# Kernel optimization log

Measured on AMD Instinct MI355X. Metric: run time of the kernel, lower is better.

## Reference

```python
import jax, jax.numpy as jnp
import numpy as np

N = 8192
D = 512
H = 256
K_TOPK = 21  # k + 1 with k = 20
EPS_NORM = 1e-12
EPS_DEG = 1e-10


def setup_inputs() -> dict:
    key = jax.random.key(0)
    ks = jax.random.split(key, 10)
    s = 0.02  # small init scale so similarities are well-behaved
    return {
        "features": jax.random.normal(ks[0], (N, D), jnp.float32),
        "masked_features": jax.random.normal(ks[1], (N, D), jnp.float32),
        "W1": jax.random.normal(ks[2], (D, D), jnp.float32) * s,
        "b1": jax.random.normal(ks[3], (D,), jnp.float32) * s,
        "W2": jax.random.normal(ks[4], (D, D), jnp.float32) * s,
        "b2": jax.random.normal(ks[5], (D,), jnp.float32) * s,
        "Wg1": jax.random.normal(ks[6], (D, H), jnp.float32) * s,
        "bg1": jax.random.normal(ks[7], (H,), jnp.float32) * s,
        "Wg2": jax.random.normal(ks[8], (H, D), jnp.float32) * s,
        "bg2": jax.random.normal(ks[9], (D,), jnp.float32) * s,
    }


def reference(features, masked_features, W1, b1, W2, b2, Wg1, bg1, Wg2, bg2):
    # ---- graph generator MLP ----
    h = jax.nn.relu(features @ W1 + b1)            # [N, D]
    emb = h @ W2 + b2                              # [N, D]
    norm = jnp.linalg.norm(emb, axis=1, keepdims=True)
    emb = emb / jnp.maximum(norm, EPS_NORM)        # F.normalize(dim=1, p=2)
    sim = emb @ emb.T                              # [N, N] cosine similarity

    # ---- top-k mask (k+1 neighbors), zero diagonal ----
    _, idx = jax.lax.top_k(sim, K_TOPK)            # [N, K]
    rows = jnp.arange(N)[:, None]
    mask = jnp.zeros((N, N), sim.dtype).at[rows, idx].set(1.0)
    mask = mask * (1.0 - jnp.eye(N, dtype=sim.dtype))  # fill_diagonal_(0)
    mask = jax.lax.stop_gradient(mask)
    sim = jax.nn.relu(sim * mask)

    # ---- symmetrize ----
    gen_adj = (sim + sim.T) * 0.5                  # [N, N]

    # ---- degree norm: D^{-1/2} (A + I) D^{-1/2} ----
    A = gen_adj + jnp.eye(N, dtype=gen_adj.dtype)
    inv_sqrt_deg = 1.0 / (jnp.sqrt(A.sum(axis=1)) + EPS_DEG)
    A = inv_sqrt_deg[:, None] * A * inv_sqrt_deg[None, :]

    # ---- two dense GCN hops (dropout inert in eval mode) ----
    h1 = jax.nn.relu(A @ (masked_features @ Wg1 + bg1))  # [N, H]
    h3 = A @ (h1 @ Wg2 + bg2)                            # [N, D]
    return h3, gen_adj
```

## Files before the change

### kernel.cpp

```cpp
#include <hip/hip_runtime.h>
#include <cstdint>
#include <cstddef>

#define NN 8192
#define DD 512
#define HH 256
#define KTOP 21
#define CCAP 192
#define CMIN 48
#define ECAP 224
#define NBIN 1024

typedef __attribute__((ext_vector_type(8))) __bf16 bf16x8;
typedef __attribute__((ext_vector_type(4))) float f32x4;

__device__ __forceinline__ unsigned short f2bf(float x) {
    unsigned u = __float_as_uint(x);
    u += 0x7fffu + ((u >> 16) & 1u);
    return (unsigned short)(u >> 16);
}
__device__ __forceinline__ float bf2f(unsigned short h) {
    return __uint_as_float(((unsigned)h) << 16);
}
__device__ __forceinline__ unsigned ordkey(float x) {
    unsigned b = __float_as_uint(x);
    return b ^ (((int)b >> 31) | 0x80000000u);
}

#define GLD16(gp, lp) __builtin_amdgcn_global_load_lds( \
    (const __attribute__((address_space(1))) unsigned int*)(gp), \
    (__attribute__((address_space(3))) unsigned int*)(lp), 16, 0, 0)

template<bool TRANSB, int ACT>
__global__ __launch_bounds__(256)
void sgemm128(const float* __restrict__ A, const float* __restrict__ B,
              const float* __restrict__ bias, float* __restrict__ C,
              int M, int N, int K) {
    constexpr int BM = 128, BN = 128, BK = 16;
    __shared__ float As[BK][BM + 4];
    __shared__ float Bs[BK][BN + 4];

    const int tiles_n = N / BN;
    const int by = blockIdx.x / tiles_n;
    const int bx = blockIdx.x % tiles_n;
    const int row0 = by * BM, col0 = bx * BN;
    const int tid = threadIdx.x;
    const int tx = tid & 15, ty = tid >> 4;

    float acc[8][8];
#pragma unroll
    for (int m = 0; m < 8; ++m)
#pragma unroll
        for (int n = 0; n < 8; ++n) acc[m][n] = 0.f;

    for (int k0 = 0; k0 < K; k0 += BK) {
#pragma unroll
        for (int l = 0; l < 2; ++l) {
            int f = tid + l * 256;
            int r = f >> 2, c4 = f & 3;
            float4 v = *reinterpret_cast<const float4*>(
                A + (size_t)(row0 + r) * K + k0 + c4 * 4);
            As[c4 * 4 + 0][r] = v.x;
            As[c4 * 4 + 1][r] = v.y;
            As[c4 * 4 + 2][r] = v.z;
            As[c4 * 4 + 3][r] = v.w;
        }
        if (TRANSB) {
#pragma unroll
            for (int l = 0; l < 2; ++l) {
                int f = tid + l * 256;
                int r = f >> 2, c4 = f & 3;
                float4 v = *reinterpret_cast<const float4*>(
                    B + (size_t)(col0 + r) * K + k0 + c4 * 4);
                Bs[c4 * 4 + 0][r] = v.x;
                Bs[c4 * 4 + 1][r] = v.y;
                Bs[c4 * 4 + 2][r] = v.z;
                Bs[c4 * 4 + 3][r] = v.w;
            }
        } else {
#pragma unroll
            for (int l = 0; l < 2; ++l) {
                int f = tid + l * 256;
                int kr = f >> 5, n4 = f & 31;
                *reinterpret_cast<float4*>(&Bs[kr][n4 * 4]) =
                    *reinterpret_cast<const float4*>(
                        B + (size_t)(k0 + kr) * N + col0 + n4 * 4);
            }
        }
        __syncthreads();

#pragma unroll
        for (int kk = 0; kk < BK; ++kk) {
            float a[8], b[8];
            *(float4*)&a[0] = *(const float4*)&As[kk][ty * 8];
            *(float4*)&a[4] = *(const float4*)&As[kk][ty * 8 + 4];
            *(float4*)&b[0] = *(const float4*)&Bs[kk][tx * 8];
            *(float4*)&b[4] = *(const float4*)&Bs[kk][tx * 8 + 4];
#pragma unroll
            for (int m = 0; m < 8; ++m)
#pragma unroll
                for (int n = 0; n < 8; ++n)
                    acc[m][n] = fmaf(a[m], b[n], acc[m][n]);
        }
        __syncthreads();
    }

    const int crow = row0 + ty * 8;
    const int ccol = col0 + tx * 8;
    float bv[8];
#pragma unroll
    for (int n = 0; n < 8; ++n) bv[n] = bias ? bias[ccol + n] : 0.f;
#pragma unroll
    for (int m = 0; m < 8; ++m) {
        float o[8];
#pragma unroll
        for (int n = 0; n < 8; ++n) {
            float t = acc[m][n] + bv[n];
            if (ACT == 1) t = fmaxf(t, 0.f);
            o[n] = t;
        }
        *reinterpret_cast<float4*>(C + (size_t)(crow + m) * N + ccol)     = *(float4*)&o[0];
        *reinterpret_cast<float4*>(C + (size_t)(crow + m) * N + ccol + 4) = *(float4*)&o[4];
    }
}

__global__ __launch_bounds__(256)
void rownorm_emit_kernel(float* __restrict__ emb, unsigned short* __restrict__ ehi) {
    const int row = blockIdx.x, tid = threadIdx.x;
    float* rp = emb + (size_t)row * DD;
    float v0 = rp[tid], v1 = rp[tid + 256];
    float sum = v0 * v0 + v1 * v1;
#pragma unroll
    for (int off = 32; off > 0; off >>= 1) sum += __shfl_down(sum, off, 64);
    __shared__ float ws[4];
    __shared__ float sc_sh;
    if ((tid & 63) == 0) ws[tid >> 6] = sum;
    __syncthreads();
    if (tid == 0) {
        float n = sqrtf(ws[0] + ws[1] + ws[2] + ws[3]);
        sc_sh = 1.0f / fmaxf(n, 1e-12f);
    }
    __syncthreads();
    float sc = sc_sh;
    v0 *= sc; v1 *= sc;
    rp[tid] = v0;
    rp[tid + 256] = v1;
    ehi[(size_t)row * DD + tid]       = f2bf(v0);
    ehi[(size_t)row * DD + tid + 256] = f2bf(v1);
}

__global__ __launch_bounds__(256)
void split_kernel(const float* __restrict__ e, unsigned short* __restrict__ hi,
                  unsigned short* __restrict__ lo) {
    const int i = (blockIdx.x * 256 + threadIdx.x) * 4;
    float4 v = *reinterpret_cast<const float4*>(e + i);
    ushort4 h, l;
    h.x = f2bf(v.x); l.x = f2bf(v.x - bf2f(h.x));
    h.y = f2bf(v.y); l.y = f2bf(v.y - bf2f(h.y));
    h.z = f2bf(v.z); l.z = f2bf(v.z - bf2f(h.z));
    h.w = f2bf(v.w); l.w = f2bf(v.w - bf2f(h.w));
    *reinterpret_cast<ushort4*>(hi + i) = h;
    *reinterpret_cast<ushort4*>(lo + i) = l;
}

__global__ __launch_bounds__(256)
void wtrans_kernel(const float* __restrict__ W, unsigned short* __restrict__ Thi,
                   unsigned short* __restrict__ Tlo, int K, int N) {
    int t = blockIdx.x * 256 + threadIdx.x;
    if (t >= K * N) return;
    int k = t / N, n = t - k * N;
    float x = W[t];
    unsigned short h = f2bf(x);
    Thi[(size_t)n * K + k] = h;
    Tlo[(size_t)n * K + k] = f2bf(x - bf2f(h));
}

__global__ __launch_bounds__(256)
void zero_kernel(float4* __restrict__ adj4, float4* __restrict__ ecnt4) {
    const float4 z = {0.f, 0.f, 0.f, 0.f};
    size_t gid = (size_t)blockIdx.x * 256 + threadIdx.x;
    const size_t stride = (size_t)gridDim.x * 256;
    const size_t total = (size_t)NN * NN / 4;
    for (size_t i = gid; i < total; i += stride) adj4[i] = z;
    if (gid < NN / 4) ecnt4[gid] = z;
}

__global__ __launch_bounds__(256)
void simgemm_bf16(const unsigned short* __restrict__ Ehi,
                  unsigned short* __restrict__ Cb) {
    const int bid = blockIdx.x;
    const int swz = (bid & 7) * 512 + (bid >> 3);
    const int by = swz >> 6, bx = swz & 63;

    __shared__ unsigned short Ah[128 * 32];
    __shared__ unsigned short Bh[128 * 32];

    const int tid = threadIdx.x, lane = tid & 63, wid = tid >> 6;
    const int wm = wid >> 1, wn = wid & 1;
    const int fr = lane & 15, fq = lane >> 4;
    const int lrow = lane >> 2;
    const int lcol8 = (lane & 3) * 8;

    const size_t arow0 = (size_t)by * 128;
    const size_t brow0 = (size_t)bx * 128;

    f32x4 acc[4][4];
#pragma unroll
    for (int m = 0; m < 4; ++m)
#pragma unroll
        for (int n = 0; n < 4; ++n) acc[m][n] = (f32x4){0.f, 0.f, 0.f, 0.f};

    for (int k0 = 0; k0 < DD; k0 += 32) {
#pragma unroll
        for (int i = 0; i < 2; ++i) {
            const int chunk = wid + i * 4;
            const int grow = chunk * 16 + lrow;
            GLD16(Ehi + (arow0 + grow) * DD + (k0 + lcol8), Ah + chunk * 512);
            GLD16(Ehi + (brow0 + grow) * DD + (k0 + lcol8), Bh + chunk * 512);
        }
        __syncthreads();

        bf16x8 ah[4], bh[4];
#pragma unroll
        for (int mf = 0; mf < 4; ++mf)
            ah[mf] = *(const bf16x8*)&Ah[(wm * 64 + mf * 16 + fr) * 32 + fq * 8];
#pragma unroll
        for (int nf = 0; nf < 4; ++nf)
            bh[nf] = *(const bf16x8*)&Bh[(wn * 64 + nf * 16 + fr) * 32 + fq * 8];
#pragma unroll
        for (int mf = 0; mf < 4; ++mf)
#pragma unroll
            for (int nf = 0; nf < 4; ++nf)
                acc[mf][nf] = __builtin_amdgcn_mfma_f32_16x16x32_bf16(ah[mf], bh[nf], acc[mf][nf], 0, 0, 0);
        __syncthreads();
    }

#pragma unroll
    for (int mf = 0; mf < 4; ++mf) {
#pragma unroll
        for (int nf = 0; nf < 4; ++nf) {
            const size_t row = arow0 + wm * 64 + mf * 16 + fq * 4;
            const int col = bx * 128 + wn * 64 + nf * 16 + fr;
#pragma unroll
            for (int r2 = 0; r2 < 4; ++r2)
                Cb[(row + r2) * NN + col] = f2bf(acc[mf][nf][r2]);
        }
    }
}

template<int KDIM>
__global__ __launch_bounds__(256)
void mfma_nt_bias(const unsigned short* __restrict__ Ahi,
                  const unsigned short* __restrict__ Alo,
                  const unsigned short* __restrict__ Bhi,
                  const unsigned short* __restrict__ Blo,
                  const float* __restrict__ bias, float* __restrict__ C, int N) {
    const int tiles_n = N / 128;
    const int by = blockIdx.x / tiles_n, bx = blockIdx.x % tiles_n;

    __shared__ unsigned short Ah[128 * 32];
    __shared__ unsigned short Al[128 * 32];
    __shared__ unsigned short Bh[128 * 32];
    __shared__ unsigned short Bl[128 * 32];

    const int tid = threadIdx.x, lane = tid & 63, wid = tid >> 6;
    const int wm = wid >> 1, wn = wid & 1;
    const int fr = lane & 15, fq = lane >> 4;
    const int lrow = lane >> 2;
    const int lcol8 = (lane & 3) * 8;

    const size_t arow0 = (size_t)by * 128;
    const size_t brow0 = (size_t)bx * 128;

    f32x4 acc[4][4];
#pragma unroll
    for (int m = 0; m < 4; ++m)
#pragma unroll
        for (int n = 0; n < 4; ++n) acc[m][n] = (f32x4){0.f, 0.f, 0.f, 0.f};

    for (int k0 = 0; k0 < KDIM; k0 += 32) {
#pragma unroll
        for (int i = 0; i < 2; ++i) {
            const int chunk = wid + i * 4;
            const int grow = chunk * 16 + lrow;
            GLD16(Ahi + (arow0 + grow) * KDIM + (k0 + lcol8), Ah + chunk * 512);
            GLD16(Alo + (arow0 + grow) * KDIM + (k0 + lcol8), Al + chunk * 512);
            GLD16(Bhi + (brow0 + grow) * KDIM + (k0 + lcol8), Bh + chunk * 512);
            GLD16(Blo + (brow0 + grow) * KDIM + (k0 + lcol8), Bl + chunk * 512);
        }
        __syncthreads();

        bf16x8 ah[4], al[4], bh[4], bl[4];
#pragma unroll
        for (int mf = 0; mf < 4; ++mf) {
            const int r = wm * 64 + mf * 16 + fr;
            ah[mf] = *(const bf16x8*)&Ah[r * 32 + fq * 8];
            al[mf] = *(const bf16x8*)&Al[r * 32 + fq * 8];
        }
#pragma unroll
        for (int nf = 0; nf < 4; ++nf) {
            const int r = wn * 64 + nf * 16 + fr;
            bh[nf] = *(const bf16x8*)&Bh[r * 32 + fq * 8];
            bl[nf] = *(const bf16x8*)&Bl[r * 32 + fq * 8];
        }
#pragma unroll
        for (int mf = 0; mf < 4; ++mf)
#pragma unroll
            for (int nf = 0; nf < 4; ++nf) {
                acc[mf][nf] = __builtin_amdgcn_mfma_f32_16x16x32_bf16(ah[mf], bh[nf], acc[mf][nf], 0, 0, 0);
                acc[mf][nf] = __builtin_amdgcn_mfma_f32_16x16x32_bf16(ah[mf], bl[nf], acc[mf][nf], 0, 0, 0);
                acc[mf][nf] = __builtin_amdgcn_mfma_f32_16x16x32_bf16(al[mf], bh[nf], acc[mf][nf], 0, 0, 0);
            }
        __syncthreads();
    }

#pragma unroll
    for (int mf = 0; mf < 4; ++mf) {
#pragma unroll
        for (int nf = 0; nf < 4; ++nf) {
            const size_t row = arow0 + wm * 64 + mf * 16 + fq * 4;
            const int col = bx * 128 + wn * 64 + nf * 16 + fr;
            const float bv = bias[col];
#pragma unroll
            for (int r2 = 0; r2 < 4; ++r2)
                C[(row + r2) * N + col] = acc[mf][nf][r2] + bv;
        }
    }
}

__global__ __launch_bounds__(256)
void topk_cand_kernel(const unsigned short* __restrict__ simb,
                      int* __restrict__ cand, int* __restrict__ ccnt) {
    const int row = blockIdx.x;
    const int tid = threadIdx.x;
    const int lane = tid & 63, wave = tid >> 6;
    const uint4* rp = reinterpret_cast<const uint4*>(simb + (size_t)row * NN);

    uint4 q[4];
#pragma unroll
    for (int t = 0; t < 4; ++t) q[t] = rp[t * 256 + tid];
    unsigned pk[16];
#pragma unroll
    for (int t = 0; t < 4; ++t) {
        pk[t * 4 + 0] = q[t].x; pk[t * 4 + 1] = q[t].y;
        pk[t * 4 + 2] = q[t].z; pk[t * 4 + 3] = q[t].w;
    }

    __shared__ int hist[NBIN];
    for (int b = tid; b < NBIN; b += 256) hist[b] = 0;
    __syncthreads();

    short bins[32];
#pragma unroll
    for (int u = 0; u < 16; ++u) {
        float flo = __uint_as_float(pk[u] << 16);
        float fhi = __uint_as_float(pk[u] & 0xFFFF0000u);
        int blo = (int)(flo * (float)NBIN); blo = max(0, min(NBIN - 1, blo));
        int bhi = (int)(fhi * (float)NBIN); bhi = max(0, min(NBIN - 1, bhi));
        bins[u * 2]     = (short)blo;
        bins[u * 2 + 1] = (short)bhi;
        atomicAdd(&hist[blo], 1);
        atomicAdd(&hist[bhi], 1);
    }
    __syncthreads();

    __shared__ int s_bstar;
    if (wave == 0) {
        int cum = 0, found = -1;
        for (int c0 = NBIN - 1; c0 >= 0 && found < 0; c0 -= 64) {
            int b = c0 - lane;
            int cnt = (b >= 0) ? hist[b] : 0;
            int sc = cnt;
#pragma unroll
            for (int off = 1; off < 64; off <<= 1) {
                int o = __shfl_up(sc, off, 64);
                if (lane >= off) sc += o;
            }
            int chunk_total = __shfl(sc, 63, 64);
            bool hit = (cum + sc >= CMIN);
            unsigned long long mh = __ballot(hit);
            if (mh) found = c0 - (__ffsll((long long)mh) - 1);
            else cum += chunk_total;
        }
        if (found < 0) found = 0;
        if (lane == 0) s_bstar = found;
    }
    __syncthreads();
    const int bstar = s_bstar;

    int cnt = 0;
#pragma unroll
    for (int i = 0; i < 32; ++i) cnt += (bins[i] >= bstar) ? 1 : 0;
    int sc = cnt;
#pragma unroll
    for (int off = 1; off < 64; off <<= 1) {
        int o = __shfl_up(sc, off, 64);
        if (lane >= off) sc += o;
    }
    __shared__ int wtot[4];
    if (lane == 63) wtot[wave] = sc;
    __syncthreads();
    int base = sc - cnt;
#pragma unroll
    for (int w = 0; w < 4; ++w)
        if (w < wave) base += wtot[w];
    int total = wtot[0] + wtot[1] + wtot[2] + wtot[3];

    int pos = base;
#pragma unroll
    for (int u = 0; u < 16; ++u) {
#pragma unroll
        for (int h = 0; h < 2; ++h) {
            if (bins[u * 2 + h] >= bstar) {
                if (pos < CCAP) {
                    int col = ((u >> 2) * 256 + tid) * 8 + (u & 3) * 2 + h;
                    cand[(size_t)row * CCAP + pos] = col;
                }
                pos++;
            }
        }
    }
    if (tid == 0) ccnt[row] = min(total, CCAP);
}

__global__ __launch_bounds__(256)
void refine_kernel(const float* __restrict__ emb, const int* __restrict__ cand,
                   const int* __restrict__ ccnt,
                   int* __restrict__ tidx, float* __restrict__ tval) {
    const int row = blockIdx.x;
    const int tid = threadIdx.x, lane = tid & 63, wv = tid >> 6;
    const int cnt = ccnt[row];
    __shared__ float sval[CCAP];
    __shared__ int   sidx[CCAP];
    const float* ei = emb + (size_t)row * DD;

    float4 a0 = reinterpret_cast<const float4*>(ei)[lane * 2];
    float4 a1 = reinterpret_cast<const float4*>(ei)[lane * 2 + 1];

    for (int base = wv * 2; base < cnt; base += 8) {
#pragma unroll
        for (int q = 0; q < 2; ++q) {
            int c = base + q;
            if (c >= cnt) break;
            const int j = cand[(size_t)row * CCAP + c];
            const float* ej = emb + (size_t)j * DD;
            float4 b0 = reinterpret_cast<const float4*>(ej)[lane * 2];
            float4 b1 = reinterpret_cast<const float4*>(ej)[lane * 2 + 1];
            float s = 0.f;
            s = fmaf(a0.x, b0.x, s); s = fmaf(a0.y, b0.y, s);
            s = fmaf(a0.z, b0.z, s); s = fmaf(a0.w, b0.w, s);
            s = fmaf(a1.x, b1.x, s); s = fmaf(a1.y, b1.y, s);
            s = fmaf(a1.z, b1.z, s); s = fmaf(a1.w, b1.w, s);
#pragma unroll
            for (int off = 32; off > 0; off >>= 1) s += __shfl_xor(s, off, 64);
            if (lane == 0) { sval[c] = s; sidx[c] = j; }
        }
    }
    __syncthreads();

    if (wv == 0) {
        float v[3]; int id[3];
#pragma unroll
        for (int k = 0; k < 3; ++k) {
            int s = lane + 64 * k;
            if (s < cnt) { v[k] = sval[s]; id[k] = sidx[s]; }
            else         { v[k] = -INFINITY; id[k] = 0x7fffffff; }
        }
#pragma unroll 1
        for (int sel = 0; sel < KTOP; ++sel) {
            float bv = v[0]; int bi = id[0];
#pragma unroll
            for (int k = 1; k < 3; ++k)
                if (v[k] > bv || (v[k] == bv && id[k] < bi)) { bv = v[k]; bi = id[k]; }
#pragma unroll
            for (int off = 1; off < 64; off <<= 1) {
                float ov = __shfl_xor(bv, off, 64);
                int   oi = __shfl_xor(bi, off, 64);
                if (ov > bv || (ov == bv && oi < bi)) { bv = ov; bi = oi; }
            }
            if (lane == 0) {
                tval[(size_t)row * KTOP + sel] = bv;
                tidx[(size_t)row * KTOP + sel] = bi;
            }
#pragma unroll
            for (int k = 0; k < 3; ++k)
                if (id[k] == bi) { v[k] = -INFINITY; id[k] = 0x7fffffff; }
        }
    }
}

__global__ __launch_bounds__(256)
void scatter_kernel(const int* __restrict__ tidx, const float* __restrict__ tval,
                    float* __restrict__ adj, int* __restrict__ ecnt,
                    int* __restrict__ ej, float* __restrict__ ev) {
    int t = blockIdx.x * 256 + threadIdx.x;
    if (t >= NN * KTOP) return;
    int i = t / KTOP;
    int j = tidx[t];
    if (j == i || j < 0) return;
    float v = tval[t];
    if (v <= 0.f) return;
    v *= 0.5f;
    atomicAdd(adj + (size_t)i * NN + j, v);
    atomicAdd(adj + (size_t)j * NN + i, v);
    int pi = atomicAdd(ecnt + i, 1);
    if (pi < ECAP) { ej[(size_t)i * ECAP + pi] = j; ev[(size_t)i * ECAP + pi] = v; }
    int pj = atomicAdd(ecnt + j, 1);
    if (pj < ECAP) { ej[(size_t)j * ECAP + pj] = i; ev[(size_t)j * ECAP + pj] = v; }
}

__global__ __launch_bounds__(256)
void sortdeg_kernel(int* __restrict__ ej, float* __restrict__ ev,
                    const int* __restrict__ ecnt, const float* __restrict__ adj,
                    float* __restrict__ sdeg) {
    const int row = blockIdx.x, tid = threadIdx.x;
    const int lane = tid & 63, wave = tid >> 6;
    const int nraw = ecnt[row];
    __shared__ float ws[4];

    if (nraw > ECAP) {
        const float4* rp = reinterpret_cast<const float4*>(adj + (size_t)row * NN);
        float sum = 0.f;
        for (int f = tid; f < NN / 4; f += 256) {
            float4 v = rp[f];
            sum += (v.x + v.y) + (v.z + v.w);
        }
#pragma unroll
        for (int off = 32; off > 0; off >>= 1) sum += __shfl_down(sum, off, 64);
        if (lane == 0) ws[wave] = sum;
        __syncthreads();
        if (tid == 0)
            sdeg[row] = 1.0f / (sqrtf(1.0f + ws[0] + ws[1] + ws[2] + ws[3]) + 1e-10f);
        return;
    }

    const int n = nraw;
    __shared__ int   lj[ECAP];
    __shared__ float lv[ECAP];
    __shared__ unsigned long long skey[ECAP];
    __shared__ int   oj[ECAP];
    __shared__ float ov[ECAP];
    if (tid < n) {
        int  jv = ej[(size_t)row * ECAP + tid];
        float vv = ev[(size_t)row * ECAP + tid];
        lj[tid] = jv; lv[tid] = vv;
        skey[tid] = ((unsigned long long)(unsigned)jv << 32) | (unsigned long long)ordkey(vv);
    }
    __syncthreads();
    if (tid < n) {
        unsigned long long mk = skey[tid];
        int rank = 0;
        for (int u = 0; u < n; ++u) {
            unsigned long long ku = skey[u];
            rank += (ku < mk || (ku == mk && u < tid)) ? 1 : 0;
        }
        oj[rank] = lj[tid];
        ov[rank] = lv[tid];
    }
    __syncthreads();
    if (tid < n) {
        ej[(size_t)row * ECAP + tid] = oj[tid];
        ev[(size_t)row * ECAP + tid] = ov[tid];
    }
    if (tid == 0) {
        float deg = 1.0f;
        for (int e = 0; e < n; ++e) deg += ov[e];
        sdeg[row] = 1.0f / (sqrtf(deg) + 1e-10f);
    }
}

template<int COLS, bool DORELU>
__global__ __launch_bounds__(256)
void spmm_edges(const int* __restrict__ ej, const float* __restrict__ ev,
                const int* __restrict__ ecnt, const float* __restrict__ adj,
                const float* __restrict__ sdeg,
                const float* __restrict__ X, float* __restrict__ Y) {
    constexpr int CPT = COLS / 256;
    const int i = blockIdx.x;
    const int tid = threadIdx.x;
    const int lane = tid & 63, wave = tid >> 6;
    const float si = sdeg[i];
    const int nraw = ecnt[i];

    float acc[CPT];
#pragma unroll
    for (int c = 0; c < CPT; ++c) acc[c] = 0.f;

    if (nraw <= ECAP) {
        __shared__ int   s_j[ECAP];
        __shared__ float s_w[ECAP];
        if (tid < nraw) {
            int j = ej[(size_t)i * ECAP + tid];
            s_j[tid] = j;
            s_w[tid] = ev[(size_t)i * ECAP + tid] * sdeg[j];
        }
        __syncthreads();
#pragma unroll 4
        for (int e = 0; e < nraw; ++e) {
            int j = s_j[e];
            float we = s_w[e];
#pragma unroll
            for (int c = 0; c < CPT; ++c)
                acc[c] += we * X[(size_t)j * COLS + tid + c * 256];
        }
    } else {
        __shared__ int   s_j[256];
        __shared__ float s_w[256];
        __shared__ int   s_cnt[4];
        const float* rowp = adj + (size_t)i * NN;
        for (int j0 = 0; j0 < NN; j0 += 256) {
            float w = rowp[j0 + tid];
            bool nz = (w != 0.f);
            unsigned long long m = __ballot(nz);
            unsigned long long ltmask = (lane == 0) ? 0ull : (~0ull >> (64 - lane));
            int pre = __popcll(m & ltmask);
            if (lane == 0) s_cnt[wave] = __popcll(m);
            __syncthreads();
            int base = 0;
#pragma unroll
            for (int q = 0; q < 4; ++q)
                if (q < wave) base += s_cnt[q];
            int total = s_cnt[0] + s_cnt[1] + s_cnt[2] + s_cnt[3];
            if (nz) {
                int p = base + pre;
                s_j[p] = j0 + tid;
                s_w[p] = w * sdeg[j0 + tid];
            }
            __syncthreads();
            for (int e = 0; e < total; ++e) {
                int j = s_j[e];
                float we = s_w[e];
#pragma unroll
                for (int c = 0; c < CPT; ++c)
                    acc[c] += we * X[(size_t)j * COLS + tid + c * 256];
            }
            __syncthreads();
        }
    }

#pragma unroll
    for (int c = 0; c < CPT; ++c) {
        float val = si * (acc[c] + si * X[(size_t)i * COLS + tid + c * 256]);
        if (DORELU) val = fmaxf(val, 0.f);
        Y[(size_t)i * COLS + tid + c * 256] = val;
    }
}

extern "C" void kernel_launch(void* const* d_in, const int* in_sizes, int n_in,
                              void* d_out, int out_size, void* d_ws, size_t ws_size,
                              hipStream_t stream) {
    const float* features = (const float*)d_in[0];
    const float* masked   = (const float*)d_in[1];
    const float* W1  = (const float*)d_in[2];
    const float* b1  = (const float*)d_in[3];
    const float* W2  = (const float*)d_in[4];
    const float* b2  = (const float*)d_in[5];
    const float* Wg1 = (const float*)d_in[6];
    const float* bg1 = (const float*)d_in[7];
    const float* Wg2 = (const float*)d_in[8];
    const float* bg2 = (const float*)d_in[9];

    float* out_h3  = (float*)d_out;
    float* out_adj = (float*)d_out + (size_t)NN * DD;
    unsigned short* simb = (unsigned short*)out_adj;

    float* Areg = (float*)d_ws;
    float* Breg = Areg + (size_t)NN * DD;
    float* tail = Breg + (size_t)NN * DD;

    float* h    = Areg;
    unsigned short* ehi = (unsigned short*)Areg;
    int*   cand = (int*)(Areg + (size_t)NN * DD / 2);
    unsigned short* mhi = (unsigned short*)Areg;
    unsigned short* mlo = mhi + (size_t)NN * DD;
    unsigned short* h1hi = (unsigned short*)Areg;
    unsigned short* h1lo = h1hi + (size_t)NN * HH;

    float* emb = Breg;
    float* x1  = Breg;
    float* h1  = Breg + (size_t)NN * HH;
    float* x2  = Breg;

    float* tval = tail;
    int*   tidx = (int*)(tval + (size_t)NN * KTOP);
    float* sdeg = (float*)(tidx + (size_t)NN * KTOP);
    int*   ecnt = (int*)(sdeg + NN);
    int*   ccnt = ecnt + NN;
    int*   elj  = ccnt + NN;
    float* elv  = (float*)(elj + (size_t)NN * ECAP);
    unsigned short* wt1hi = (unsigned short*)(elv + (size_t)NN * ECAP);
    unsigned short* wt1lo = wt1hi + (size_t)HH * DD;
    unsigned short* wt2hi = wt1lo + (size_t)HH * DD;
    unsigned short* wt2lo = wt2hi + (size_t)DD * HH;

    dim3 blk(256);

    sgemm128<false, 1><<<dim3((NN / 128) * (DD / 128)), blk, 0, stream>>>(
        features, W1, b1, h, NN, DD, DD);
    sgemm128<false, 0><<<dim3((NN / 128) * (DD / 128)), blk, 0, stream>>>(
        h, W2, b2, emb, NN, DD, DD);
    rownorm_emit_kernel<<<dim3(NN), blk, 0, stream>>>(emb, ehi);
    simgemm_bf16<<<dim3(4096), blk, 0, stream>>>(ehi, simb);
    topk_cand_kernel<<<dim3(NN), blk, 0, stream>>>(simb, cand, ccnt);
    refine_kernel<<<dim3(NN), blk, 0, stream>>>(emb, cand, ccnt, tidx, tval);
    zero_kernel<<<dim3(2048), blk, 0, stream>>>(
        (float4*)out_adj, (float4*)ecnt);
    scatter_kernel<<<dim3((NN * KTOP + 255) / 256), blk, 0, stream>>>(
        tidx, tval, out_adj, ecnt, elj, elv);
    sortdeg_kernel<<<dim3(NN), blk, 0, stream>>>(elj, elv, ecnt, out_adj, sdeg);
    split_kernel<<<dim3(NN * DD / 1024), blk, 0, stream>>>(masked, mhi, mlo);
    wtrans_kernel<<<dim3(DD * HH / 256), blk, 0, stream>>>(Wg1, wt1hi, wt1lo, DD, HH);
    mfma_nt_bias<DD><<<dim3((NN / 128) * (HH / 128)), blk, 0, stream>>>(
        mhi, mlo, wt1hi, wt1lo, bg1, x1, HH);
    spmm_edges<HH, true><<<dim3(NN), blk, 0, stream>>>(
        elj, elv, ecnt, out_adj, sdeg, x1, h1);
    split_kernel<<<dim3(NN * HH / 1024), blk, 0, stream>>>(h1, h1hi, h1lo);
    wtrans_kernel<<<dim3(HH * DD / 256), blk, 0, stream>>>(Wg2, wt2hi, wt2lo, HH, DD);
    mfma_nt_bias<HH><<<dim3((NN / 128) * (DD / 128)), blk, 0, stream>>>(
        h1hi, h1lo, wt2hi, wt2lo, bg2, x2, DD);
    spmm_edges<DD, false><<<dim3(NN), blk, 0, stream>>>(
        elj, elv, ecnt, out_adj, sdeg, x2, out_h3);
}
```

Baseline: 754.8 us.

## Fuse top-k candidate and refine, build adjacency rows in shared memory

Merges the candidate-selection and refine kernels so candidates stay in shared memory, and folds edge-list construction into the same kernel. The separate 256MB zero pass and global atomic scatter into the dense adjacency are replaced by a paint kernel that builds each row in an LDS buffer and writes it once while computing the degree. Launch count and global atomics drop. The cost is a 32KB LDS row buffer per block, which may limit occupancy, plus a very slow fallback path for rows that overflow the edge cap.

After: 1.062 ms. +40.8%, slower.

```diff
diff --git a/kernel.cpp b/kernel.cpp
--- a/kernel.cpp
+++ b/kernel.cpp
@@ -176,16 +176,6 @@
 }
 
 __global__ __launch_bounds__(256)
-void zero_kernel(float4* __restrict__ adj4, float4* __restrict__ ecnt4) {
-    const float4 z = {0.f, 0.f, 0.f, 0.f};
-    size_t gid = (size_t)blockIdx.x * 256 + threadIdx.x;
-    const size_t stride = (size_t)gridDim.x * 256;
-    const size_t total = (size_t)NN * NN / 4;
-    for (size_t i = gid; i < total; i += stride) adj4[i] = z;
-    if (gid < NN / 4) ecnt4[gid] = z;
-}
-
-__global__ __launch_bounds__(256)
 void simgemm_bf16(const unsigned short* __restrict__ Ehi,
                   unsigned short* __restrict__ Cb) {
     const int bid = blockIdx.x;
@@ -329,13 +319,16 @@
 }
 
 __global__ __launch_bounds__(256)
-void topk_cand_kernel(const unsigned short* __restrict__ simb,
-                      int* __restrict__ cand, int* __restrict__ ccnt) {
+void topk_refine_kernel(const unsigned short* __restrict__ simb,
+                        const float* __restrict__ emb,
+                        int* __restrict__ tidx, float* __restrict__ tval,
+                        int* __restrict__ ecnt, int* __restrict__ elj,
+                        float* __restrict__ elv) {
     const int row = blockIdx.x;
     const int tid = threadIdx.x;
     const int lane = tid & 63, wave = tid >> 6;
+
     const uint4* rp = reinterpret_cast<const uint4*>(simb + (size_t)row * NN);
-
     uint4 q[4];
 #pragma unroll
     for (int t = 0; t < 4; ++t) q[t] = rp[t * 256 + tid];
@@ -388,6 +381,7 @@
     __syncthreads();
     const int bstar = s_bstar;
 
+    __shared__ int s_cand[CCAP];
     int cnt = 0;
 #pragma unroll
     for (int i = 0; i < 32; ++i) cnt += (bins[i] >= bstar) ? 1 : 0;
@@ -412,37 +406,27 @@
 #pragma unroll
         for (int h = 0; h < 2; ++h) {
             if (bins[u * 2 + h] >= bstar) {
-                if (pos < CCAP) {
-                    int col = ((u >> 2) * 256 + tid) * 8 + (u & 3) * 2 + h;
-                    cand[(size_t)row * CCAP + pos] = col;
-                }
+                if (pos < CCAP)
+                    s_cand[pos] = ((u >> 2) * 256 + tid) * 8 + (u & 3) * 2 + h;
                 pos++;
             }
         }
     }
-    if (tid == 0) ccnt[row] = min(total, CCAP);
-}
-
-__global__ __launch_bounds__(256)
-void refine_kernel(const float* __restrict__ emb, const int* __restrict__ cand,
-                   const int* __restrict__ ccnt,
-                   int* __restrict__ tidx, float* __restrict__ tval) {
-    const int row = blockIdx.x;
-    const int tid = threadIdx.x, lane = tid & 63, wv = tid >> 6;
-    const int cnt = ccnt[row];
+    __syncthreads();
+    const int ncand = min(total, CCAP);
+
     __shared__ float sval[CCAP];
     __shared__ int   sidx[CCAP];
     const float* ei = emb + (size_t)row * DD;
-
     float4 a0 = reinterpret_cast<const float4*>(ei)[lane * 2];
     float4 a1 = reinterpret_cast<const float4*>(ei)[lane * 2 + 1];
 
-    for (int base = wv * 2; base < cnt; base += 8) {
-#pragma unroll
-        for (int q = 0; q < 2; ++q) {
-            int c = base + q;
-            if (c >= cnt) break;
-            const int j = cand[(size_t)row * CCAP + c];
+    for (int base2 = wave * 2; base2 < ncand; base2 += 8) {
+#pragma unroll
+        for (int qq = 0; qq < 2; ++qq) {
+            int c = base2 + qq;
+            if (c >= ncand) break;
+            const int j = s_cand[c];
             const float* ej = emb + (size_t)j * DD;
             float4 b0 = reinterpret_cast<const float4*>(ej)[lane * 2];
             float4 b1 = reinterpret_cast<const float4*>(ej)[lane * 2 + 1];
@@ -458,13 +442,15 @@
     }
     __syncthreads();
 
-    if (wv == 0) {
+    __shared__ float selv[KTOP];
+    __shared__ int   seli[KTOP];
+    if (wave == 0) {
         float v[3]; int id[3];
 #pragma unroll
         for (int k = 0; k < 3; ++k) {
             int s = lane + 64 * k;
-            if (s < cnt) { v[k] = sval[s]; id[k] = sidx[s]; }
-            else         { v[k] = -INFINITY; id[k] = 0x7fffffff; }
+            if (s < ncand) { v[k] = sval[s]; id[k] = sidx[s]; }
+            else           { v[k] = -INFINITY; id[k] = 0x7fffffff; }
         }
 #pragma unroll 1
         for (int sel = 0; sel < KTOP; ++sel) {
@@ -478,61 +464,35 @@
                 int   oi = __shfl_xor(bi, off, 64);
                 if (ov > bv || (ov == bv && oi < bi)) { bv = ov; bi = oi; }
             }
-            if (lane == 0) {
-                tval[(size_t)row * KTOP + sel] = bv;
-                tidx[(size_t)row * KTOP + sel] = bi;
-            }
+            if (lane == 0) { selv[sel] = bv; seli[sel] = bi; }
 #pragma unroll
             for (int k = 0; k < 3; ++k)
                 if (id[k] == bi) { v[k] = -INFINITY; id[k] = 0x7fffffff; }
         }
     }
-}
-
-__global__ __launch_bounds__(256)
-void scatter_kernel(const int* __restrict__ tidx, const float* __restrict__ tval,
-                    float* __restrict__ adj, int* __restrict__ ecnt,
-                    int* __restrict__ ej, float* __restrict__ ev) {
-    int t = blockIdx.x * 256 + threadIdx.x;
-    if (t >= NN * KTOP) return;
-    int i = t / KTOP;
-    int j = tidx[t];
-    if (j == i || j < 0) return;
-    float v = tval[t];
-    if (v <= 0.f) return;
-    v *= 0.5f;
-    atomicAdd(adj + (size_t)i * NN + j, v);
-    atomicAdd(adj + (size_t)j * NN + i, v);
-    int pi = atomicAdd(ecnt + i, 1);
-    if (pi < ECAP) { ej[(size_t)i * ECAP + pi] = j; ev[(size_t)i * ECAP + pi] = v; }
-    int pj = atomicAdd(ecnt + j, 1);
-    if (pj < ECAP) { ej[(size_t)j * ECAP + pj] = i; ev[(size_t)j * ECAP + pj] = v; }
-}
-
-__global__ __launch_bounds__(256)
-void sortdeg_kernel(int* __restrict__ ej, float* __restrict__ ev,
-                    const int* __restrict__ ecnt, const float* __restrict__ adj,
-                    float* __restrict__ sdeg) {
+    __syncthreads();
+
+    if (tid < KTOP) {
+        float bv = selv[tid];
+        int   bi = seli[tid];
+        tval[(size_t)row * KTOP + tid] = bv;
+        tidx[(size_t)row * KTOP + tid] = bi;
+        if (bi != row && bi >= 0 && bi < NN && bv > 0.f) {
+            float v = bv * 0.5f;
+            int pi = atomicAdd(ecnt + row, 1);
+            if (pi < ECAP) { elj[(size_t)row * ECAP + pi] = bi; elv[(size_t)row * ECAP + pi] = v; }
+            int pj = atomicAdd(ecnt + bi, 1);
+            if (pj < ECAP) { elj[(size_t)bi * ECAP + pj] = row; elv[(size_t)bi * ECAP + pj] = v; }
+        }
+    }
+}
+
+__global__ __launch_bounds__(256)
+void sort_kernel(int* __restrict__ ej, float* __restrict__ ev,
+                 const int* __restrict__ ecnt) {
     const int row = blockIdx.x, tid = threadIdx.x;
-    const int lane = tid & 63, wave = tid >> 6;
     const int nraw = ecnt[row];
-    __shared__ float ws[4];
-
-    if (nraw > ECAP) {
-        const float4* rp = reinterpret_cast<const float4*>(adj + (size_t)row * NN);
-        float sum = 0.f;
-        for (int f = tid; f < NN / 4; f += 256) {
-            float4 v = rp[f];
-            sum += (v.x + v.y) + (v.z + v.w);
-        }
-#pragma unroll
-        for (int off = 32; off > 0; off >>= 1) sum += __shfl_down(sum, off, 64);
-        if (lane == 0) ws[wave] = sum;
-        __syncthreads();
-        if (tid == 0)
-            sdeg[row] = 1.0f / (sqrtf(1.0f + ws[0] + ws[1] + ws[2] + ws[3]) + 1e-10f);
-        return;
-    }
+    if (nraw > ECAP) return;
 
     const int n = nraw;
     __shared__ int   lj[ECAP];
@@ -562,11 +522,51 @@
         ej[(size_t)row * ECAP + tid] = oj[tid];
         ev[(size_t)row * ECAP + tid] = ov[tid];
     }
-    if (tid == 0) {
-        float deg = 1.0f;
-        for (int e = 0; e < n; ++e) deg += ov[e];
-        sdeg[row] = 1.0f / (sqrtf(deg) + 1e-10f);
-    }
+}
+
+__global__ __launch_bounds__(256)
+void paint_kernel(const int* __restrict__ ej, const float* __restrict__ ev,
+                  const int* __restrict__ ecnt,
+                  const int* __restrict__ tidx, const float* __restrict__ tval,
+                  float* __restrict__ adj, float* __restrict__ sdeg) {
+    const int row = blockIdx.x, tid = threadIdx.x;
+    const int lane = tid & 63, wave = tid >> 6;
+    __shared__ float rowbuf[NN];
+    for (int c = tid; c < NN; c += 256) rowbuf[c] = 0.f;
+    __syncthreads();
+
+    const int nraw = ecnt[row];
+    if (nraw <= ECAP) {
+        for (int e = tid; e < nraw; e += 256)
+            atomicAdd(&rowbuf[ej[(size_t)row * ECAP + e]], ev[(size_t)row * ECAP + e]);
+    } else {
+        for (int t = tid; t < NN * KTOP; t += 256) {
+            int i = t / KTOP;
+            int j = tidx[t];
+            float v = tval[t];
+            if (j < 0 || j == i || v <= 0.f) continue;
+            v *= 0.5f;
+            if (i == row) atomicAdd(&rowbuf[j], v);
+            if (j == row) atomicAdd(&rowbuf[i], v);
+        }
+    }
+    __syncthreads();
+
+    float sum = 0.f;
+    float4* out4 = reinterpret_cast<float4*>(adj + (size_t)row * NN);
+    const float4* rb4 = reinterpret_cast<const float4*>(rowbuf);
+    for (int f = tid; f < NN / 4; f += 256) {
+        float4 v = rb4[f];
+        out4[f] = v;
+        sum += (v.x + v.y) + (v.z + v.w);
+    }
+#pragma unroll
+    for (int off = 32; off > 0; off >>= 1) sum += __shfl_down(sum, off, 64);
+    __shared__ float ws[4];
+    if (lane == 0) ws[wave] = sum;
+    __syncthreads();
+    if (tid == 0)
+        sdeg[row] = 1.0f / (sqrtf(1.0f + ws[0] + ws[1] + ws[2] + ws[3]) + 1e-10f);
 }
 
 template<int COLS, bool DORELU>
@@ -670,7 +670,6 @@
 
     float* h    = Areg;
     unsigned short* ehi = (unsigned short*)Areg;
-    int*   cand = (int*)(Areg + (size_t)NN * DD / 2);
     unsigned short* mhi = (unsigned short*)Areg;
     unsigned short* mlo = mhi + (size_t)NN * DD;
     unsigned short* h1hi = (unsigned short*)Areg;
@@ -685,8 +684,7 @@
     int*   tidx = (int*)(tval + (size_t)NN * KTOP);
     float* sdeg = (float*)(tidx + (size_t)NN * KTOP);
     int*   ecnt = (int*)(sdeg + NN);
-    int*   ccnt = ecnt + NN;
-    int*   elj  = ccnt + NN;
+    int*   elj  = ecnt + NN;
     float* elv  = (float*)(elj + (size_t)NN * ECAP);
     unsigned short* wt1hi = (unsigned short*)(elv + (size_t)NN * ECAP);
     unsigned short* wt1lo = wt1hi + (size_t)HH * DD;
@@ -701,13 +699,12 @@
         h, W2, b2, emb, NN, DD, DD);
     rownorm_emit_kernel<<<dim3(NN), blk, 0, stream>>>(emb, ehi);
     simgemm_bf16<<<dim3(4096), blk, 0, stream>>>(ehi, simb);
-    topk_cand_kernel<<<dim3(NN), blk, 0, stream>>>(simb, cand, ccnt);
-    refine_kernel<<<dim3(NN), blk, 0, stream>>>(emb, cand, ccnt, tidx, tval);
-    zero_kernel<<<dim3(2048), blk, 0, stream>>>(
-        (float4*)out_adj, (float4*)ecnt);
-    scatter_kernel<<<dim3((NN * KTOP + 255) / 256), blk, 0, stream>>>(
-        tidx, tval, out_adj, ecnt, elj, elv);
-    sortdeg_kernel<<<dim3(NN), blk, 0, stream>>>(elj, elv, ecnt, out_adj, sdeg);
+    hipMemsetAsync(ecnt, 0, (size_t)NN * sizeof(int), stream);
+    topk_refine_kernel<<<dim3(NN), blk, 0, stream>>>(
+        simb, emb, tidx, tval, ecnt, elj, elv);
+    sort_kernel<<<dim3(NN), blk, 0, stream>>>(elj, elv, ecnt);
+    paint_kernel<<<dim3(NN), blk, 0, stream>>>(
+        elj, elv, ecnt, tidx, tval, out_adj, sdeg);
     split_kernel<<<dim3(NN * DD / 1024), blk, 0, stream>>>(masked, mhi, mlo);
     wtrans_kernel<<<dim3(DD * HH / 256), blk, 0, stream>>>(Wg1, wt1hi, wt1lo, DD, HH);
     mfma_nt_bias<DD><<<dim3((NN / 128) * (HH / 128)), blk, 0, stream>>>(
```
